# Performance work log

Hardware: AMD Instinct MI355X
Metric: run time of the kernel (lower is better)

Reference implementation:

```python
import jax, jax.numpy as jnp
import numpy as np

N = 50000      # nodes
E = 800000     # edges
D_IN, D_HID, D_OUT = 1433, 64, 7
EPS = 1e-7       # eps[float32] in hgcn Hyperboloid
MIN_NORM = 1e-15
MAX_NORM = 1e6
# c = 1 -> K = 1/c = 1, sqrtK = 1 (folded into constants below)


def proj(x):
    # reset time coordinate so point lies on the hyperboloid
    y = x[:, 1:]
    y_sqnorm = jnp.sum(y * y, axis=1, keepdims=True)
    x0 = jnp.sqrt(jnp.clip(1.0 + y_sqnorm, EPS))
    return jnp.concatenate([x0, y], axis=1)


def proj_tan0(u):
    return jnp.concatenate([jnp.zeros_like(u[:, :1]), u[:, 1:]], axis=1)


def expmap0(u):
    x = u[:, 1:]
    x_norm = jnp.clip(jnp.linalg.norm(x, axis=1, keepdims=True), MIN_NORM)
    theta = x_norm
    res = jnp.concatenate([jnp.cosh(theta), jnp.sinh(theta) * x / x_norm], axis=1)
    return proj(res)


def logmap0(x):
    y = x[:, 1:]
    y_norm = jnp.clip(jnp.linalg.norm(y, axis=1, keepdims=True), MIN_NORM)
    theta = jnp.clip(x[:, :1], 1.0 + EPS)
    return jnp.concatenate([jnp.zeros_like(theta), jnp.arccosh(theta) * y / y_norm], axis=1)


def minkowski_dot(x, y):
    return jnp.sum(x * y, axis=-1, keepdims=True) - 2.0 * x[:, :1] * y[:, :1]


def proj_tan(u, x):
    ux = jnp.sum(x[:, 1:] * u[:, 1:], axis=1, keepdims=True)
    v0 = ux / jnp.clip(x[:, :1], EPS)
    return jnp.concatenate([v0, u[:, 1:]], axis=1)


def expmap(u, x):
    normu = jnp.sqrt(jnp.clip(minkowski_dot(u, u), EPS))
    normu = jnp.minimum(normu, MAX_NORM)
    theta = jnp.clip(normu, MIN_NORM)
    result = jnp.cosh(theta) * x + jnp.sinh(theta) * u / theta
    return proj(result)


def ptransp0(x, u):
    x0, y = x[:, :1], x[:, 1:]
    y_norm = jnp.clip(jnp.linalg.norm(y, axis=1, keepdims=True), MIN_NORM)
    yn = y / y_norm
    v = jnp.concatenate([-y_norm, (1.0 - x0) * yn], axis=1)
    alpha = jnp.sum(yn * u[:, 1:], axis=1, keepdims=True)
    return proj_tan(u - alpha * v, x)


def mobius_add(x, y):
    u = logmap0(y)
    v = ptransp0(x, u)
    return expmap(v, x)


def hyp_linear(x, W, b):
    # mobius_matvec then hyperbolic bias add (dropout=0)
    mv = expmap0(logmap0(x) @ W.T)
    res = proj(mv)
    hyp_bias = proj(expmap0(proj_tan0(b[None, :])))
    return proj(mobius_add(res, hyp_bias))


def hyp_agg(x, row, col, edge_weight):
    # spmm(adj, logmap0(x)) via edge-list scatter-add
    xt = logmap0(x)
    msg = edge_weight[:, None] * xt[col]          # [E, d]
    support = jax.ops.segment_sum(msg, row, num_segments=N)
    return proj(expmap0(support))


def hyp_act(x):
    xt = jax.nn.relu(logmap0(x))
    xt = proj_tan0(xt)
    return proj(expmap0(xt))


def setup_inputs() -> dict:
    key = jax.random.key(0)
    ks = jax.random.split(key, 8)
    return {
        "x": jax.random.normal(ks[0], (N, D_IN), dtype=jnp.float32),
        "row": jax.random.randint(ks[1], (E,), 0, N),
        "col": jax.random.randint(ks[2], (E,), 0, N),
        "edge_weight": jax.random.uniform(ks[3], (E,), dtype=jnp.float32) * 0.1,
        "W1": jax.random.normal(ks[4], (D_HID, D_IN), dtype=jnp.float32) * 0.02,
        "b1": jax.random.normal(ks[5], (D_HID,), dtype=jnp.float32) * 0.02,
        "W2": jax.random.normal(ks[6], (D_OUT, D_HID), dtype=jnp.float32) * 0.05,
        "b2": jax.random.normal(ks[7], (D_OUT,), dtype=jnp.float32) * 0.02,
    }


def reference(x, row, col, edge_weight, W1, b1, W2, b2):
    # map features to the hyperboloid
    x_hyp = proj(expmap0(proj_tan0(x)))
    # layer 1: HypLinear -> HypAgg -> HypAct
    h = hyp_act(hyp_agg(hyp_linear(x_hyp, W1, b1), row, col, edge_weight))
    # layer 2
    h = hyp_act(hyp_agg(hyp_linear(h, W2, b2), row, col, edge_weight))
    # back to tangent space at origin
    return proj_tan0(logmap0(h))
```

## Files before the change

kernel.cpp:

```cpp
#include <hip/hip_runtime.h>
#include <hip/hip_bf16.h>

#define NN 50000
#define EE 800000
#define DIN 1433
#define KTOT 1432
#define KHALF 716
#define NKT 23
#define NB 196
#define EPSC 1e-7f
#define MINN 1e-15f
#define MAXN 1e6f

typedef __attribute__((ext_vector_type(8))) short bf16x8;
typedef __attribute__((ext_vector_type(4))) float f32x4;

#define WF_OFF     0
#define Z1A_OFF    94208
#define Z1B_OFF    (Z1A_OFF + 3200000)
#define XT3_OFF    (Z1B_OFF + 3200000)
#define CNT_OFF    (XT3_OFF + 400000)
#define ROWPTR_OFF (CNT_OFF + 50000)
#define CUR_OFF    (ROWPTR_OFF + 50002)
#define BSUM_OFF   (CUR_OFF + 50000)
#define BOFF_OFF   (BSUM_OFF + 256)
#define UB_OFF     (BOFF_OFF + 256)
#define EP_OFF     (UB_OFF + 128)

__device__ __forceinline__ float wsum(float v) {
#pragma unroll
  for (int o = 1; o < 64; o <<= 1) v += __shfl_xor(v, o, 64);
  return v;
}

__device__ __forceinline__ float gsum8(float v) {
#pragma unroll
  for (int o = 1; o < 8; o <<= 1) v += __shfl_xor(v, o, 64);
  return v;
}

__device__ __forceinline__ void split_bf(float v, unsigned int& hbits16, unsigned int& lbits16) {
  unsigned int b = __float_as_uint(v);
  unsigned int hb = b & 0xFFFF0000u;
  float r = v - __uint_as_float(hb);
  unsigned int lb = __float_as_uint(r);
  lbits16 = (lb + 0x7FFFu + ((lb >> 16) & 1u)) >> 16;
  hbits16 = hb >> 16;
}

__device__ __forceinline__ float fsinh(float x) {
  float e = __expf(x);
  return 0.5f * (e - __fdividef(1.f, e));
}
__device__ __forceinline__ float facoshp(float z) {
  return __logf(z + sqrtf(fmaxf(z * z - 1.f, 0.f)));
}

__device__ float bias_tangent(const float* b, int lane, int D) {
  const bool sp = (lane >= 1) && (lane < D);
  float bsp = sp ? b[lane] : 0.f;
  float rb = fmaxf(sqrtf(wsum(bsp * bsp)), MINN);
  float bsh = fsinh(rb);
  float hb = sp ? bsh * __fdividef(bsp, rb) : 0.f;
  float hbn2 = wsum(hb * hb);
  float hb0 = sqrtf(fmaxf(1.f + hbn2, EPSC));
  float hbyn = fmaxf(sqrtf(hbn2), MINN);
  return sp ? facoshp(fmaxf(hb0, 1.f + EPSC)) * __fdividef(hb, hbyn) : 0.f;
}

__device__ float chain_with_u(float z, float u, int lane, int D) {
  const bool sp = (lane >= 1) && (lane < D);
  float s = sp ? z : 0.f;
  float r = fmaxf(sqrtf(wsum(s * s)), MINN);
  float sh = fsinh(r);
  float y = sp ? sh * __fdividef(s, r) : 0.f;
  float yn2 = wsum(y * y);
  float x0 = sqrtf(fmaxf(1.f + yn2, EPSC));
  float y_norm = fmaxf(sqrtf(yn2), MINN);
  float ynv = sp ? __fdividef(y, y_norm) : 0.f;
  float alpha = wsum(ynv * u);
  float wsp = sp ? u - alpha * (1.f - x0) * ynv : 0.f;
  float ux = wsum(y * wsp);
  float v0 = __fdividef(ux, fmaxf(x0, EPSC));
  float vt = (lane == 0) ? v0 : wsp;
  float md = wsum(vt * vt) - 2.f * v0 * v0;
  float nu = sqrtf(fmaxf(md, EPSC));
  nu = fminf(nu, MAXN);
  float th = fmaxf(nu, MINN);
  float e = __expf(th), ei = __fdividef(1.f, e);
  float cth = 0.5f * (e + ei), sth = 0.5f * (e - ei);
  float resx = (lane == 0) ? x0 : y;
  float eres = fmaf(cth, resx, sth * __fdividef(vt, th));
  float en2 = wsum(sp ? eres * eres : 0.f);
  float e0 = sqrtf(fmaxf(1.f + en2, EPSC));
  float eyn = fmaxf(sqrtf(en2), MINN);
  return sp ? facoshp(fmaxf(e0, 1.f + EPSC)) * __fdividef(eres, eyn) : 0.f;
}

__device__ float agg_act_chain(float sin_, int lane, int D) {
  const bool sp = (lane >= 1) && (lane < D);
  float s = sp ? sin_ : 0.f;
  float r = fmaxf(sqrtf(wsum(s * s)), MINN);
  float sh = fsinh(r);
  float g = sp ? sh * __fdividef(s, r) : 0.f;
  float gn2 = wsum(g * g);
  float g0 = sqrtf(fmaxf(1.f + gn2, EPSC));
  float gyn = fmaxf(sqrtf(gn2), MINN);
  float l = sp ? facoshp(fmaxf(g0, 1.f + EPSC)) * __fdividef(g, gyn) : 0.f;
  float t = fmaxf(l, 0.f);
  float rt = fmaxf(sqrtf(wsum(t * t)), MINN);
  float sht = fsinh(rt);
  float h = sp ? sht * __fdividef(t, rt) : 0.f;
  float hn2 = wsum(h * h);
  float h0 = sqrtf(fmaxf(1.f + hn2, EPSC));
  float hyn = fmaxf(sqrtf(hn2), MINN);
  return sp ? facoshp(fmaxf(h0, 1.f + EPSC)) * __fdividef(h, hyn) : 0.f;
}

__device__ float agg_act_chain8(float sin_, int f) {
  const bool sp = (f >= 1) && (f < 7);
  float s = sp ? sin_ : 0.f;
  float r = fmaxf(sqrtf(gsum8(s * s)), MINN);
  float sh = fsinh(r);
  float g = sp ? sh * __fdividef(s, r) : 0.f;
  float gn2 = gsum8(g * g);
  float g0 = sqrtf(fmaxf(1.f + gn2, EPSC));
  float gyn = fmaxf(sqrtf(gn2), MINN);
  float l = sp ? facoshp(fmaxf(g0, 1.f + EPSC)) * __fdividef(g, gyn) : 0.f;
  float t = fmaxf(l, 0.f);
  float rt = fmaxf(sqrtf(gsum8(t * t)), MINN);
  float sht = fsinh(rt);
  float h = sp ? sht * __fdividef(t, rt) : 0.f;
  float hn2 = gsum8(h * h);
  float h0 = sqrtf(fmaxf(1.f + hn2, EPSC));
  float hyn = fmaxf(sqrtf(hn2), MINN);
  return sp ? facoshp(fmaxf(h0, 1.f + EPSC)) * __fdividef(h, hyn) : 0.f;
}

__global__ __launch_bounds__(128) void prep_bias(const float* __restrict__ b1,
                                                 const float* __restrict__ b2,
                                                 float* __restrict__ ub) {
  const int w = threadIdx.x >> 6, lane = threadIdx.x & 63;
  if (w == 0) ub[lane] = bias_tangent(b1, lane, 64);
  else        ub[64 + lane] = bias_tangent(b2, lane, 7);
}

__global__ __launch_bounds__(256) void prep_wfrag(const float* __restrict__ W1,
                                                  unsigned short* __restrict__ wfrag) {
  int idx = blockIdx.x * 256 + threadIdx.x;
  if (idx >= 2 * NKT * 8 * 64) return;
  int lane = idx & 63;
  int c = (idx >> 6) & 7;
  int rest = idx >> 9;
  int kt = rest % NKT;
  int half = rest / NKT;
  int type = c >> 2, nt = c & 3;
  int col = nt * 16 + (lane & 15);
  unsigned short vals[8];
#pragma unroll
  for (int i = 0; i < 8; ++i) {
    int lk = kt * 32 + (lane >> 4) * 8 + i;
    float wv = (lk < KHALF) ? W1[col * DIN + half * KHALF + lk + 1] : 0.f;
    unsigned int h16, l16;
    split_bf(wv, h16, l16);
    vals[i] = (unsigned short)((type == 0) ? h16 : l16);
  }
  unsigned short* dst = wfrag + (((size_t)(half * NKT + kt) * 8 + c) * 64 + lane) * 8;
#pragma unroll
  for (int i = 0; i < 8; ++i) dst[i] = vals[i];
}

__global__ __launch_bounds__(256) void gemm_half(const float* __restrict__ x,
                                                 const unsigned short* __restrict__ wfrag,
                                                 float* __restrict__ z) {
  __shared__ __align__(16) unsigned short Ah[32][40];
  __shared__ __align__(16) unsigned short Al[32][40];
  __shared__ __align__(16) unsigned short Bf[8][64][8];
  const int tid = threadIdx.x;
  const int w = tid >> 6, lane = tid & 63;
  const int row0 = blockIdx.x * 32;
  const int half = blockIdx.y;
  const unsigned short* wf = wfrag + (size_t)half * NKT * 4096;
  float* zp = z + (size_t)half * 3200000;

  f32x4 acc[2];
  acc[0] = (f32x4){0.f, 0.f, 0.f, 0.f};
  acc[1] = (f32x4){0.f, 0.f, 0.f, 0.f};

  const int lrow = tid >> 3;
  const int kq = (tid & 7) * 4;
  const int gr = row0 + lrow;
  const bool rok = (gr < NN);
  const float* __restrict__ xr = x + (size_t)gr * DIN + 1 + half * KHALF;

  const int nt0 = (w >> 1) * 2;

  float v[4];
#pragma unroll
  for (int j = 0; j < 4; ++j) v[j] = rok ? xr[kq + j] : 0.f;

  for (int kt = 0; kt < NKT; ++kt) {
    __builtin_amdgcn_sched_barrier(0);
    asm volatile("s_waitcnt lgkmcnt(0)" ::: "memory");
    __builtin_amdgcn_s_barrier();
    __builtin_amdgcn_sched_barrier(0);
    {
      unsigned int h[4], l[4];
#pragma unroll
      for (int j = 0; j < 4; ++j) split_bf(v[j], h[j], l[j]);
      uint2 hw, lw;
      hw.x = h[0] | (h[1] << 16); hw.y = h[2] | (h[3] << 16);
      lw.x = l[0] | (l[1] << 16); lw.y = l[2] | (l[3] << 16);
      *(uint2*)&Ah[lrow][kq] = hw;
      *(uint2*)&Al[lrow][kq] = lw;
    }
    if (w == 0) {
      const unsigned short* src = wf + (size_t)kt * 4096 + lane * 8;
#pragma unroll
      for (int c = 0; c < 8; ++c) {
        __builtin_amdgcn_global_load_lds(
            (const __attribute__((address_space(1))) unsigned int*)(src + c * 512),
            (__attribute__((address_space(3))) unsigned int*)(&Bf[c][0][0]),
            16, 0, 0);
      }
    }
    __builtin_amdgcn_sched_barrier(0);
    asm volatile("s_waitcnt vmcnt(0) lgkmcnt(0)" ::: "memory");
    __builtin_amdgcn_s_barrier();
    __builtin_amdgcn_sched_barrier(0);
    if (kt + 1 < NKT) {
      const int k0n = (kt + 1) * 32;
#pragma unroll
      for (int j = 0; j < 4; ++j) {
        int lk = k0n + kq + j;
        v[j] = (rok && lk < KHALF) ? xr[lk] : 0.f;
      }
    }
    const int arow = (w & 1) * 16 + (lane & 15);
    const int kb = (lane >> 4) * 8;
    bf16x8 ah = *(const bf16x8*)&Ah[arow][kb];
    bf16x8 al = *(const bf16x8*)&Al[arow][kb];
    bf16x8 bh[2], bl[2];
#pragma unroll
    for (int n = 0; n < 2; ++n) {
      bh[n] = *(const bf16x8*)&Bf[nt0 + n][lane][0];
      bl[n] = *(const bf16x8*)&Bf[4 + nt0 + n][lane][0];
    }
#pragma unroll
    for (int n = 0; n < 2; ++n) {
      acc[n] = __builtin_amdgcn_mfma_f32_16x16x32_bf16(ah, bh[n], acc[n], 0, 0, 0);
      acc[n] = __builtin_amdgcn_mfma_f32_16x16x32_bf16(ah, bl[n], acc[n], 0, 0, 0);
      acc[n] = __builtin_amdgcn_mfma_f32_16x16x32_bf16(al, bh[n], acc[n], 0, 0, 0);
    }
  }
#pragma unroll
  for (int n = 0; n < 2; ++n)
#pragma unroll
    for (int i = 0; i < 4; ++i) {
      int orow = row0 + (w & 1) * 16 + (lane >> 4) * 4 + i;
      int ocol = (nt0 + n) * 16 + (lane & 15);
      if (orow < NN) zp[(size_t)orow * 64 + ocol] = acc[n][i];
    }
}

__global__ __launch_bounds__(256) void node1(const float* __restrict__ z1a,
                                             const float* __restrict__ z1b,
                                             const float* __restrict__ ub, float* xt) {
  const int node = blockIdx.x * 4 + (threadIdx.x >> 6);
  const int lane = threadIdx.x & 63;
  const int idx = node * 64 + lane;
  float z = z1a[idx] + z1b[idx];
  float u1 = ub[lane];
  float o = chain_with_u(z, u1, lane, 64);
  xt[idx] = o;
}

__global__ __launch_bounds__(256) void k_zero(int* __restrict__ cnt) {
  int i = blockIdx.x * 256 + threadIdx.x;
  if (i < NN) cnt[i] = 0;
}

__global__ __launch_bounds__(256) void k_hist(const int* __restrict__ row, int* __restrict__ cnt) {
  int e = blockIdx.x * 256 + threadIdx.x;
  if (e < EE) atomicAdd(&cnt[row[e]], 1);
}

__global__ __launch_bounds__(256) void k_blocksum(const int* __restrict__ cnt,
                                                  int* __restrict__ bsum) {
  __shared__ int wpart[4];
  int i = blockIdx.x * 256 + threadIdx.x;
  int v = (i < NN) ? cnt[i] : 0;
  int s = v;
#pragma unroll
  for (int o = 1; o < 64; o <<= 1) s += __shfl_xor(s, o, 64);
  if ((threadIdx.x & 63) == 0) wpart[threadIdx.x >> 6] = s;
  __syncthreads();
  if (threadIdx.x == 0) bsum[blockIdx.x] = wpart[0] + wpart[1] + wpart[2] + wpart[3];
}

__global__ __launch_bounds__(256) void k_scanb(const int* __restrict__ bsum,
                                               int* __restrict__ boff) {
  __shared__ int s[256];
  int t = threadIdx.x;
  int v = (t < NB) ? bsum[t] : 0;
  s[t] = v;
  __syncthreads();
  for (int o = 1; o < 256; o <<= 1) {
    int a = (t >= o) ? s[t - o] : 0;
    __syncthreads();
    s[t] += a;
    __syncthreads();
  }
  if (t < NB) boff[t] = s[t] - v;
}

__global__ __launch_bounds__(256) void k_apply(const int* __restrict__ cnt,
                                               const int* __restrict__ boff,
                                               int* __restrict__ rowptr, int* __restrict__ cur) {
  __shared__ int s[256];
  int i = blockIdx.x * 256 + threadIdx.x;
  int t = threadIdx.x;
  int v = (i < NN) ? cnt[i] : 0;
  s[t] = v;
  __syncthreads();
  for (int o = 1; o < 256; o <<= 1) {
    int a = (t >= o) ? s[t - o] : 0;
    __syncthreads();
    s[t] += a;
    __syncthreads();
  }
  int ex = s[t] - v + boff[blockIdx.x];
  if (i < NN) { rowptr[i] = ex; cur[i] = ex; }
  if (i == NN - 1) rowptr[NN] = EE;
}

__global__ __launch_bounds__(256) void k_scatter(const int* __restrict__ row,
                                                 const int* __restrict__ col,
                                                 const float* __restrict__ ew,
                                                 int* __restrict__ cur, uint2* __restrict__ ep) {
  int e = blockIdx.x * 256 + threadIdx.x;
  if (e < EE) {
    int p = atomicAdd(&cur[row[e]], 1);
    uint2 q;
    q.x = (unsigned int)col[e];
    q.y = __float_as_uint(ew[e]);
    ep[p] = q;
  }
}

__global__ __launch_bounds__(256) void agg1_node2(const int* __restrict__ rowptr,
                                                  const uint2* __restrict__ ep,
                                                  const float* __restrict__ xt,
                                                  const float* __restrict__ W2,
                                                  const float* __restrict__ ub,
                                                  float* __restrict__ xt3) {
  const int node = blockIdx.x * 4 + (threadIdx.x >> 6);
  const int lane = threadIdx.x & 63;
  const int s0 = rowptr[node], s1 = rowptr[node + 1];
  float a0 = 0.f, a1 = 0.f, a2 = 0.f, a3 = 0.f;
  float a4 = 0.f, a5 = 0.f, a6 = 0.f, a7 = 0.f;
  int p = s0;
  for (; p + 8 <= s1; p += 8) {
    uint2 q0 = ep[p], q1 = ep[p + 1], q2 = ep[p + 2], q3 = ep[p + 3];
    uint2 q4 = ep[p + 4], q5 = ep[p + 5], q6 = ep[p + 6], q7 = ep[p + 7];
    a0 = fmaf(__uint_as_float(q0.y), xt[(size_t)q0.x * 64 + lane], a0);
    a1 = fmaf(__uint_as_float(q1.y), xt[(size_t)q1.x * 64 + lane], a1);
    a2 = fmaf(__uint_as_float(q2.y), xt[(size_t)q2.x * 64 + lane], a2);
    a3 = fmaf(__uint_as_float(q3.y), xt[(size_t)q3.x * 64 + lane], a3);
    a4 = fmaf(__uint_as_float(q4.y), xt[(size_t)q4.x * 64 + lane], a4);
    a5 = fmaf(__uint_as_float(q5.y), xt[(size_t)q5.x * 64 + lane], a5);
    a6 = fmaf(__uint_as_float(q6.y), xt[(size_t)q6.x * 64 + lane], a6);
    a7 = fmaf(__uint_as_float(q7.y), xt[(size_t)q7.x * 64 + lane], a7);
  }
  for (; p < s1; ++p) {
    uint2 q = ep[p];
    a0 = fmaf(__uint_as_float(q.y), xt[(size_t)q.x * 64 + lane], a0);
  }
  float acc = ((a0 + a1) + (a2 + a3)) + ((a4 + a5) + (a6 + a7));
  float xt2 = agg_act_chain(acc, lane, 64);
  float z2 = 0.f;
#pragma unroll
  for (int jj = 1; jj < 7; ++jj) {
    float wv = W2[jj * 64 + lane];
    float sjj = wsum(xt2 * wv);
    if (lane == jj) z2 = sjj;
  }
  float u2 = ub[64 + lane];
  float o = chain_with_u(z2, u2, lane, 7);
  if (lane < 8) xt3[node * 8 + lane] = o;
}

__global__ __launch_bounds__(256) void agg2_final(const int* __restrict__ rowptr,
                                                  const uint2* __restrict__ ep,
                                                  const float* __restrict__ xt3,
                                                  float* __restrict__ out) {
  const int node = blockIdx.x * 32 + (threadIdx.x >> 3);
  const int f = threadIdx.x & 7;
  const int nc = (node < NN) ? node : (NN - 1);
  const int s0 = rowptr[nc], s1 = rowptr[nc + 1];
  float a0 = 0.f, a1 = 0.f, a2 = 0.f, a3 = 0.f;
  int p = s0;
  for (; p + 4 <= s1; p += 4) {
    uint2 q0 = ep[p], q1 = ep[p + 1], q2 = ep[p + 2], q3 = ep[p + 3];
    a0 = fmaf(__uint_as_float(q0.y), xt3[(size_t)q0.x * 8 + f], a0);
    a1 = fmaf(__uint_as_float(q1.y), xt3[(size_t)q1.x * 8 + f], a1);
    a2 = fmaf(__uint_as_float(q2.y), xt3[(size_t)q2.x * 8 + f], a2);
    a3 = fmaf(__uint_as_float(q3.y), xt3[(size_t)q3.x * 8 + f], a3);
  }
  for (; p < s1; ++p) {
    uint2 q = ep[p];
    a0 = fmaf(__uint_as_float(q.y), xt3[(size_t)q.x * 8 + f], a0);
  }
  float acc = (a0 + a1) + (a2 + a3);
  float o = agg_act_chain8(acc, f);
  if (node < NN && f < 7) out[node * 7 + f] = o;
}

extern "C" void kernel_launch(void* const* d_in, const int* in_sizes, int n_in,
                              void* d_out, int out_size, void* d_ws, size_t ws_size,
                              hipStream_t stream) {
  const float* x = (const float*)d_in[0];
  const int* row = (const int*)d_in[1];
  const int* col = (const int*)d_in[2];
  const float* ew = (const float*)d_in[3];
  const float* W1 = (const float*)d_in[4];
  const float* b1 = (const float*)d_in[5];
  const float* W2 = (const float*)d_in[6];
  const float* b2 = (const float*)d_in[7];
  float* ws = (float*)d_ws;
  unsigned short* wfrag = (unsigned short*)(ws + WF_OFF);
  float* z1a = ws + Z1A_OFF;
  float* z1b = ws + Z1B_OFF;
  float* xt3 = ws + XT3_OFF;
  int* cnt = (int*)(ws + CNT_OFF);
  int* rowptr = (int*)(ws + ROWPTR_OFF);
  int* cur = (int*)(ws + CUR_OFF);
  int* bsum = (int*)(ws + BSUM_OFF);
  int* boff = (int*)(ws + BOFF_OFF);
  float* ub = ws + UB_OFF;
  uint2* ep = (uint2*)(ws + EP_OFF);
  float* out = (float*)d_out;

  k_zero<<<dim3(NB), dim3(256), 0, stream>>>(cnt);
  k_hist<<<dim3(3125), dim3(256), 0, stream>>>(row, cnt);
  k_blocksum<<<dim3(NB), dim3(256), 0, stream>>>(cnt, bsum);
  k_scanb<<<dim3(1), dim3(256), 0, stream>>>(bsum, boff);
  k_apply<<<dim3(NB), dim3(256), 0, stream>>>(cnt, boff, rowptr, cur);
  k_scatter<<<dim3(3125), dim3(256), 0, stream>>>(row, col, ew, cur, ep);

  prep_bias<<<dim3(1), dim3(128), 0, stream>>>(b1, b2, ub);
  prep_wfrag<<<dim3(92), dim3(256), 0, stream>>>(W1, wfrag);
  gemm_half<<<dim3(1563, 2), dim3(256), 0, stream>>>(x, wfrag, z1a);
  node1<<<dim3(12500), dim3(256), 0, stream>>>(z1a, z1b, ub, z1a);

  agg1_node2<<<dim3(12500), dim3(256), 0, stream>>>(rowptr, ep, z1a, W2, ub, xt3);
  agg2_final<<<dim3(1563), dim3(256), 0, stream>>>(rowptr, ep, xt3, out);
}
```

Before: 328.9 us.

## Pipeline first-layer GEMM with async LDS staging of X and weight fragments

The first-layer GEMM now copies raw fp32 X tiles straight into LDS with async global-to-LDS loads. X uses a triple buffer with an XOR-swizzled layout, and the weight fragments use a double buffer whose loads are spread across all four waves. The bf16 hi/lo split moves to after the LDS read, and the per-tile barriers wait with partial vmcnt so the next tiles' loads overlap the current MFMAs. This removes the serial register-load, split, store and barrier sequence and the single-wave B load. In exchange, tail K tiles are no longer masked: they read neighbouring X values, relying on the zero-padded weights, and the last row may read slightly past the end of the buffer.

Result: faster. 305.3 us (-7.2%).

```diff
diff --git a/kernel.cpp b/kernel.cpp
--- a/kernel.cpp
+++ b/kernel.cpp
@@ -173,84 +173,89 @@
 __global__ __launch_bounds__(256) void gemm_half(const float* __restrict__ x,
                                                  const unsigned short* __restrict__ wfrag,
                                                  float* __restrict__ z) {
-  __shared__ __align__(16) unsigned short Ah[32][40];
-  __shared__ __align__(16) unsigned short Al[32][40];
-  __shared__ __align__(16) unsigned short Bf[8][64][8];
+  __shared__ __align__(16) float XA[3 * 1024];
+  __shared__ __align__(16) unsigned short BB[2][8][64][8];
   const int tid = threadIdx.x;
   const int w = tid >> 6, lane = tid & 63;
   const int row0 = blockIdx.x * 32;
   const int half = blockIdx.y;
   const unsigned short* wf = wfrag + (size_t)half * NKT * 4096;
   float* zp = z + (size_t)half * 3200000;
+  const int nt0 = (w >> 1) * 2;
+
+  auto stageB = [&](int kt, int p) {
+    const unsigned short* src = wf + (size_t)kt * 4096 + (2 * w) * 512 + lane * 8;
+    __builtin_amdgcn_global_load_lds(
+        (const __attribute__((address_space(1))) unsigned int*)src,
+        (__attribute__((address_space(3))) unsigned int*)(&BB[p][2 * w][0][0]), 16, 0, 0);
+    __builtin_amdgcn_global_load_lds(
+        (const __attribute__((address_space(1))) unsigned int*)(src + 512),
+        (__attribute__((address_space(3))) unsigned int*)(&BB[p][2 * w + 1][0][0]), 16, 0, 0);
+  };
+  auto stageA = [&](int kt, int q) {
+#pragma unroll
+    for (int i = 0; i < 4; ++i) {
+      int fi = (w * 4 + i) * 64 + lane;
+      int r = fi >> 5, pk = fi & 31;
+      int lb = (pk >> 2) ^ (r & 7);
+      int grow = row0 + r; if (grow >= NN) grow = NN - 1;
+      const float* src = x + (size_t)grow * DIN + 1 + half * KHALF + kt * 32 + lb * 4 + (pk & 3);
+      __builtin_amdgcn_global_load_lds(
+          (const __attribute__((address_space(1))) unsigned int*)src,
+          (__attribute__((address_space(3))) unsigned int*)(XA + q * 1024 + (w * 4 + i) * 64),
+          4, 0, 0);
+    }
+  };
 
   f32x4 acc[2];
   acc[0] = (f32x4){0.f, 0.f, 0.f, 0.f};
   acc[1] = (f32x4){0.f, 0.f, 0.f, 0.f};
 
-  const int lrow = tid >> 3;
-  const int kq = (tid & 7) * 4;
-  const int gr = row0 + lrow;
-  const bool rok = (gr < NN);
-  const float* __restrict__ xr = x + (size_t)gr * DIN + 1 + half * KHALF;
-
-  const int nt0 = (w >> 1) * 2;
-
-  float v[4];
-#pragma unroll
-  for (int j = 0; j < 4; ++j) v[j] = rok ? xr[kq + j] : 0.f;
+  stageB(0, 0);
+  stageA(0, 0);
+  stageA(1, 1);
+  __builtin_amdgcn_sched_barrier(0);
+  asm volatile("s_waitcnt vmcnt(4)" ::: "memory");
+  __builtin_amdgcn_s_barrier();
+  __builtin_amdgcn_sched_barrier(0);
+
+  const int rr = (w & 1) * 16 + (lane & 15);
+  const int b0 = (lane >> 4) * 2;
+  const int pb0 = (b0 ^ (rr & 7)) * 4;
+  const int pb1 = ((b0 + 1) ^ (rr & 7)) * 4;
 
   for (int kt = 0; kt < NKT; ++kt) {
-    __builtin_amdgcn_sched_barrier(0);
-    asm volatile("s_waitcnt lgkmcnt(0)" ::: "memory");
-    __builtin_amdgcn_s_barrier();
-    __builtin_amdgcn_sched_barrier(0);
-    {
-      unsigned int h[4], l[4];
-#pragma unroll
-      for (int j = 0; j < 4; ++j) split_bf(v[j], h[j], l[j]);
-      uint2 hw, lw;
-      hw.x = h[0] | (h[1] << 16); hw.y = h[2] | (h[3] << 16);
-      lw.x = l[0] | (l[1] << 16); lw.y = l[2] | (l[3] << 16);
-      *(uint2*)&Ah[lrow][kq] = hw;
-      *(uint2*)&Al[lrow][kq] = lw;
-    }
-    if (w == 0) {
-      const unsigned short* src = wf + (size_t)kt * 4096 + lane * 8;
-#pragma unroll
-      for (int c = 0; c < 8; ++c) {
-        __builtin_amdgcn_global_load_lds(
-            (const __attribute__((address_space(1))) unsigned int*)(src + c * 512),
-            (__attribute__((address_space(3))) unsigned int*)(&Bf[c][0][0]),
-            16, 0, 0);
-      }
-    }
-    __builtin_amdgcn_sched_barrier(0);
-    asm volatile("s_waitcnt vmcnt(0) lgkmcnt(0)" ::: "memory");
-    __builtin_amdgcn_s_barrier();
-    __builtin_amdgcn_sched_barrier(0);
-    if (kt + 1 < NKT) {
-      const int k0n = (kt + 1) * 32;
-#pragma unroll
-      for (int j = 0; j < 4; ++j) {
-        int lk = k0n + kq + j;
-        v[j] = (rok && lk < KHALF) ? xr[lk] : 0.f;
-      }
-    }
-    const int arow = (w & 1) * 16 + (lane & 15);
-    const int kb = (lane >> 4) * 8;
-    bf16x8 ah = *(const bf16x8*)&Ah[arow][kb];
-    bf16x8 al = *(const bf16x8*)&Al[arow][kb];
+    if (kt + 1 < NKT) stageB(kt + 1, (kt + 1) & 1);
+    if (kt + 2 < NKT) stageA(kt + 2, (kt + 2) % 3);
+    const float* xa = XA + (kt % 3) * 1024 + rr * 32;
+    float4 f0 = *(const float4*)(xa + pb0);
+    float4 f1 = *(const float4*)(xa + pb1);
+    float af[8] = {f0.x, f0.y, f0.z, f0.w, f1.x, f1.y, f1.z, f1.w};
+    unsigned int h[8], l[8];
+#pragma unroll
+    for (int j = 0; j < 8; ++j) split_bf(af[j], h[j], l[j]);
+    bf16x8 ah, al;
+#pragma unroll
+    for (int j = 0; j < 8; ++j) { ah[j] = (short)h[j]; al[j] = (short)l[j]; }
     bf16x8 bh[2], bl[2];
 #pragma unroll
     for (int n = 0; n < 2; ++n) {
-      bh[n] = *(const bf16x8*)&Bf[nt0 + n][lane][0];
-      bl[n] = *(const bf16x8*)&Bf[4 + nt0 + n][lane][0];
+      bh[n] = *(const bf16x8*)&BB[kt & 1][nt0 + n][lane][0];
+      bl[n] = *(const bf16x8*)&BB[kt & 1][4 + nt0 + n][lane][0];
     }
 #pragma unroll
     for (int n = 0; n < 2; ++n) {
       acc[n] = __builtin_amdgcn_mfma_f32_16x16x32_bf16(ah, bh[n], acc[n], 0, 0, 0);
       acc[n] = __builtin_amdgcn_mfma_f32_16x16x32_bf16(ah, bl[n], acc[n], 0, 0, 0);
       acc[n] = __builtin_amdgcn_mfma_f32_16x16x32_bf16(al, bh[n], acc[n], 0, 0, 0);
+    }
+    if (kt + 1 < NKT) {
+      __builtin_amdgcn_sched_barrier(0);
+      asm volatile("s_waitcnt lgkmcnt(0)" ::: "memory");
+      if (kt + 2 < NKT) asm volatile("s_waitcnt vmcnt(4)" ::: "memory");
+      else              asm volatile("s_waitcnt vmcnt(0)" ::: "memory");
+      __builtin_amdgcn_s_barrier();
+      __builtin_amdgcn_sched_barrier(0);
     }
   }
 #pragma unroll
```
